# Optimization experiments

Hardware: AMD Instinct MI355X
Metric: run time of the kernel (lower is better)

The kernel has to match this reference:

```python
import jax, jax.numpy as jnp
import numpy as np

VAR_CXCY = 0.1   # SSD encoding variances
VAR_WH = 0.2
THRESH = 0.5     # match threshold from forward()
EPS = 1e-6


def point_form(p):
    """[P,4] (cx,cy,w,h) -> (x1,y1,x2,y2)."""
    return jnp.concatenate([p[..., :2] - p[..., 2:] / 2,
                            p[..., :2] + p[..., 2:] / 2], axis=-1)


def iou(a, b):
    """a: [N,4] xyxy, b: [P,4] xyxy -> [N,P] jaccard overlap."""
    lt = jnp.maximum(a[:, None, :2], b[None, :, :2])
    rb = jnp.minimum(a[:, None, 2:], b[None, :, 2:])
    wh = jnp.clip(rb - lt, 0.0)
    inter = wh[..., 0] * wh[..., 1]
    area_a = (a[:, 2] - a[:, 0]) * (a[:, 3] - a[:, 1])
    area_b = (b[:, 2] - b[:, 0]) * (b[:, 3] - b[:, 1])
    return inter / (area_a[:, None] + area_b[None, :] - inter + EPS)


def match_one(gt, labels, priors, priors_pt):
    """SSD match for a single image.
    gt: [N,4] xyxy, labels: [N] int, priors: [P,4] cxcywh, priors_pt: [P,4] xyxy.
    Returns loc targets [P,4] and conf targets [P] (0 = background).
    """
    ov = iou(gt, priors_pt)                       # [N,P]
    best_prior_idx = jnp.argmax(ov, axis=1)        # [N] best prior per gt
    best_truth_ov = jnp.max(ov, axis=0)            # [P]
    best_truth_idx = jnp.argmax(ov, axis=0)        # [P] best gt per prior
    n = gt.shape[0]
    # ensure every gt keeps its best prior
    best_truth_ov = best_truth_ov.at[best_prior_idx].set(2.0)
    best_truth_idx = best_truth_idx.at[best_prior_idx].set(jnp.arange(n))
    matches = gt[best_truth_idx]                   # [P,4]
    conf = labels[best_truth_idx] + 1              # shift so 0 = background
    conf = jnp.where(best_truth_ov < THRESH, 0, conf)
    # encode matched boxes relative to priors
    m_cxcy = (matches[:, :2] + matches[:, 2:]) * 0.5
    m_wh = jnp.clip(matches[:, 2:] - matches[:, :2], EPS)
    g_cxcy = (m_cxcy - priors[:, :2]) / (VAR_CXCY * priors[:, 2:])
    g_wh = jnp.log(m_wh / priors[:, 2:]) / VAR_WH
    return jnp.concatenate([g_cxcy, g_wh], axis=1), conf


def setup_inputs() -> dict:
    key = jax.random.key(0)
    k1, k2, k3, k4, k5 = jax.random.split(key, 5)
    B, N, P = 32, 100, 8732
    # ground-truth boxes: valid xyxy corners in [0,1]
    xy1 = jax.random.uniform(k1, (B, N, 2)) * 0.7
    wh = 0.05 + jax.random.uniform(k2, (B, N, 2)) * 0.25
    gt_boxes = jnp.concatenate([xy1, xy1 + wh], axis=-1).astype(jnp.float32)
    gt_labels = jax.random.randint(k3, (B, N), 0, 20)
    # priors: cxcywh
    p_cxcy = jax.random.uniform(k4, (P, 2))
    p_wh = 0.05 + jax.random.uniform(k5, (P, 2)) * 0.45
    priors = jnp.concatenate([p_cxcy, p_wh], axis=-1).astype(jnp.float32)
    return {"gt_boxes": gt_boxes, "gt_labels": gt_labels, "priors": priors}


def reference(gt_boxes, gt_labels, priors):
    priors_pt = point_form(priors)
    loc_t, conf_t = jax.vmap(
        lambda g, l: match_one(g, l, priors, priors_pt))(gt_boxes, gt_labels)
    return loc_t, conf_t
```

## Files before the change

### kernel.cpp

```cpp
#include <hip/hip_runtime.h>

#pragma clang fp contract(off)

#define BB 32
#define NN 100
#define PP 8732

__global__ __launch_bounds__(256) void k_iou_pass(
    const float* __restrict__ gt,
    const float* __restrict__ priors,
    unsigned long long* __restrict__ gkey,
    unsigned char* __restrict__ m8)
{
    __shared__ float4 s_gt[NN];
    __shared__ float  s_area[NN];
    __shared__ unsigned long long s_rk[4][NN];

    const int b    = blockIdx.y;
    const int t    = threadIdx.x;
    const int lane = t & 63;
    const int wid  = t >> 6;
    const int p    = blockIdx.x * 256 + t;
    const bool valid = p < PP;

    if (t < NN) {
        float4 g = reinterpret_cast<const float4*>(gt)[b * NN + t];
        s_gt[t] = g;
        s_area[t] = (g.z - g.x) * (g.w - g.y);
    }
    __syncthreads();

    const int pc = valid ? p : (PP - 1);
    const float4 pr = reinterpret_cast<const float4*>(priors)[pc];
    const float px1 = pr.x - pr.z * 0.5f;
    const float py1 = pr.y - pr.w * 0.5f;
    const float px2 = pr.x + pr.z * 0.5f;
    const float py2 = pr.y + pr.w * 0.5f;
    const float area_b = (px2 - px1) * (py2 - py1);

    float best_ov = -1.0f;
    int best_j = 0;

    #pragma unroll 2
    for (int j = 0; j < NN; ++j) {
        float4 g = s_gt[j];
        float ltx = fmaxf(g.x, px1), lty = fmaxf(g.y, py1);
        float rbx = fminf(g.z, px2), rby = fminf(g.w, py2);
        float w = fmaxf(rbx - ltx, 0.0f), h = fmaxf(rby - lty, 0.0f);
        float inter = w * h;
        float iou = inter / (s_area[j] + area_b - inter + 1e-6f);
        if (!valid) iou = -1.0f;

        if (iou > best_ov) { best_ov = iou; best_j = j; }

        float wm = iou;
        for (int off = 32; off; off >>= 1)
            wm = fmaxf(wm, __shfl_xor(wm, off));
        unsigned long long mask = __ballot(iou == wm);
        if (lane == __ffsll((unsigned long long)mask) - 1) {
            s_rk[wid][j] = (wm >= 0.0f)
                ? (((unsigned long long)__float_as_uint(wm) << 32) |
                   (unsigned int)(~p))
                : 0ull;
        }
    }
    __syncthreads();

    if (t < NN) {
        unsigned long long k0 = s_rk[0][t], k1 = s_rk[1][t];
        unsigned long long k2 = s_rk[2][t], k3 = s_rk[3][t];
        unsigned long long ka = k0 > k1 ? k0 : k1;
        unsigned long long kb = k2 > k3 ? k2 : k3;
        unsigned long long k  = ka > kb ? ka : kb;
        atomicMax(&gkey[b * NN + t], k);
    }
    if (valid) {
        m8[b * PP + p] =
            (unsigned char)(best_j | ((best_ov < 0.5f) ? 0x80 : 0));
    }
}

__global__ __launch_bounds__(256) void k_encode(
    const float* __restrict__ gt,
    const int*   __restrict__ labels,
    const float* __restrict__ priors,
    const unsigned long long* __restrict__ gkey,
    const unsigned char* __restrict__ m8,
    float* __restrict__ loc_out,
    float* __restrict__ conf_out)
{
    __shared__ float4 s_gt[NN];
    __shared__ int    s_lab[NN];
    __shared__ int    s_kp[NN];

    const int b = blockIdx.y;
    const int t = threadIdx.x;
    if (t < NN) {
        s_gt[t] = reinterpret_cast<const float4*>(gt)[b * NN + t];
        s_lab[t] = labels[b * NN + t];
        unsigned int lo = (unsigned int)(gkey[b * NN + t] & 0xFFFFFFFFull);
        s_kp[t] = (int)(~lo);
    }
    __syncthreads();

    const int p = blockIdx.x * 256 + t;
    if (p >= PP) return;

    int forced_j = -1;
    #pragma unroll 4
    for (int j = 0; j < NN; ++j)
        if (s_kp[j] == p) forced_j = j;

    const unsigned char m = m8[b * PP + p];
    const int j    = (forced_j >= 0) ? forced_j : (m & 0x7f);
    const int conf = (forced_j < 0 && (m & 0x80)) ? 0 : (s_lab[j] + 1);

    const float4 pr = reinterpret_cast<const float4*>(priors)[p];
    const float4 g  = s_gt[j];
    const float mcx = (g.x + g.z) * 0.5f;
    const float mcy = (g.y + g.w) * 0.5f;
    const float mw  = fmaxf(g.z - g.x, 1e-6f);
    const float mh  = fmaxf(g.w - g.y, 1e-6f);
    const float gcx = (mcx - pr.x) / (0.1f * pr.z);
    const float gcy = (mcy - pr.y) / (0.1f * pr.w);
    const float gw  = logf(mw / pr.z) / 0.2f;
    const float gh  = logf(mh / pr.w) / 0.2f;

    reinterpret_cast<float4*>(loc_out)[b * PP + p] =
        make_float4(gcx, gcy, gw, gh);
    conf_out[b * PP + p] = (float)conf;
}

extern "C" void kernel_launch(void* const* d_in, const int* in_sizes, int n_in,
                              void* d_out, int out_size, void* d_ws, size_t ws_size,
                              hipStream_t stream) {
    const float* gt     = (const float*)d_in[0];
    const int*   labels = (const int*)  d_in[1];
    const float* priors = (const float*)d_in[2];

    float* loc  = (float*)d_out;
    float* conf = (float*)d_out + (size_t)BB * PP * 4;

    unsigned long long* gkey = (unsigned long long*)d_ws;
    unsigned char* m8 = (unsigned char*)d_ws + (size_t)BB * NN * 8;

    hipMemsetAsync(gkey, 0, (size_t)BB * NN * 8, stream);

    dim3 grid((PP + 255) / 256, BB);
    k_iou_pass<<<grid, 256, 0, stream>>>(gt, priors, gkey, m8);
    k_encode<<<grid, 256, 0, stream>>>(gt, labels, priors, gkey, m8, loc, conf);
}
```

Baseline: 117.6 us.

## Replace per-gt wave shuffle reductions with chunked shared-memory IoU column reduction

The IoU pass no longer does a 6-step shuffle max plus ballot for each of the 100 ground-truth boxes. It writes IoU values for 16 gt boxes at a time into a padded shared-memory tile, then reduces each gt column with a two-level scan over 16-element segments, followed by an atomicMax. Ground-truth boxes are now read directly from global memory (uniform loads) rather than staged in shared memory, and the encode kernel likewise drops its shared-memory staging in favour of direct global reads. This trades shuffle and ballot work for extra barriers per chunk and serial shared-memory scans. Invalid priors now produce IoU 0 instead of -1, which relies on tie-breaking by prior index favouring valid lanes.

```diff
diff --git a/kernel.cpp b/kernel.cpp
--- a/kernel.cpp
+++ b/kernel.cpp
@@ -5,6 +5,8 @@
 #define BB 32
 #define NN 100
 #define PP 8732
+#define CH 16
+#define LDW 257
 
 __global__ __launch_bounds__(256) void k_iou_pass(
     const float* __restrict__ gt,
@@ -12,25 +14,15 @@
     unsigned long long* __restrict__ gkey,
     unsigned char* __restrict__ m8)
 {
-    __shared__ float4 s_gt[NN];
-    __shared__ float  s_area[NN];
-    __shared__ unsigned long long s_rk[4][NN];
+    __shared__ unsigned int s_iou[CH * LDW];
+    __shared__ unsigned long long s_part[CH][17];
 
-    const int b    = blockIdx.y;
-    const int t    = threadIdx.x;
-    const int lane = t & 63;
-    const int wid  = t >> 6;
-    const int p    = blockIdx.x * 256 + t;
+    const int b = blockIdx.y;
+    const int t = threadIdx.x;
+    const int p = blockIdx.x * 256 + t;
     const bool valid = p < PP;
+    const int pc = valid ? p : (PP - 1);
 
-    if (t < NN) {
-        float4 g = reinterpret_cast<const float4*>(gt)[b * NN + t];
-        s_gt[t] = g;
-        s_area[t] = (g.z - g.x) * (g.w - g.y);
-    }
-    __syncthreads();
-
-    const int pc = valid ? p : (PP - 1);
     const float4 pr = reinterpret_cast<const float4*>(priors)[pc];
     const float px1 = pr.x - pr.z * 0.5f;
     const float py1 = pr.y - pr.w * 0.5f;
@@ -38,42 +30,62 @@
     const float py2 = pr.y + pr.w * 0.5f;
     const float area_b = (px2 - px1) * (py2 - py1);
 
+    const float4* __restrict__ gtb =
+        reinterpret_cast<const float4*>(gt) + b * NN;
+
     float best_ov = -1.0f;
     int best_j = 0;
 
-    #pragma unroll 2
-    for (int j = 0; j < NN; ++j) {
-        float4 g = s_gt[j];
-        float ltx = fmaxf(g.x, px1), lty = fmaxf(g.y, py1);
-        float rbx = fminf(g.z, px2), rby = fminf(g.w, py2);
-        float w = fmaxf(rbx - ltx, 0.0f), h = fmaxf(rby - lty, 0.0f);
-        float inter = w * h;
-        float iou = inter / (s_area[j] + area_b - inter + 1e-6f);
-        if (!valid) iou = -1.0f;
+    for (int jc = 0; jc < NN; jc += CH) {
+        const int nr = min(NN - jc, CH);
 
-        if (iou > best_ov) { best_ov = iou; best_j = j; }
+        #pragma unroll 4
+        for (int jj = 0; jj < nr; ++jj) {
+            const int j = jc + jj;
+            float4 g = gtb[j];
+            float area_a = (g.z - g.x) * (g.w - g.y);
+            float ltx = fmaxf(g.x, px1), lty = fmaxf(g.y, py1);
+            float rbx = fminf(g.z, px2), rby = fminf(g.w, py2);
+            float w = fmaxf(rbx - ltx, 0.0f), h = fmaxf(rby - lty, 0.0f);
+            float inter = w * h;
+            float iou = inter / (area_a + area_b - inter + 1e-6f);
+            if (!valid) iou = 0.0f;
+            if (iou > best_ov) { best_ov = iou; best_j = j; }
+            s_iou[jj * LDW + t] = __float_as_uint(iou);
+        }
+        __syncthreads();
 
-        float wm = iou;
-        for (int off = 32; off; off >>= 1)
-            wm = fmaxf(wm, __shfl_xor(wm, off));
-        unsigned long long mask = __ballot(iou == wm);
-        if (lane == __ffsll((unsigned long long)mask) - 1) {
-            s_rk[wid][j] = (wm >= 0.0f)
-                ? (((unsigned long long)__float_as_uint(wm) << 32) |
-                   (unsigned int)(~p))
-                : 0ull;
+        {
+            const int r = t & 15;
+            const int s = t >> 4;
+            if (r < nr) {
+                const unsigned int* row = s_iou + r * LDW + s * 16;
+                unsigned int bb = row[0];
+                int bi = 0;
+                #pragma unroll
+                for (int i = 1; i < 16; ++i) {
+                    unsigned int v = row[i];
+                    if (v > bb) { bb = v; bi = i; }
+                }
+                int pw = blockIdx.x * 256 + s * 16 + bi;
+                s_part[r][s] = ((unsigned long long)bb << 32) |
+                               (unsigned int)(~pw);
+            }
         }
+        __syncthreads();
+
+        if (t < nr) {
+            unsigned long long best = s_part[t][0];
+            #pragma unroll
+            for (int s = 1; s < 16; ++s) {
+                unsigned long long k = s_part[t][s];
+                if (k > best) best = k;
+            }
+            atomicMax(&gkey[b * NN + jc + t], best);
+        }
+        __syncthreads();
     }
-    __syncthreads();
 
-    if (t < NN) {
-        unsigned long long k0 = s_rk[0][t], k1 = s_rk[1][t];
-        unsigned long long k2 = s_rk[2][t], k3 = s_rk[3][t];
-        unsigned long long ka = k0 > k1 ? k0 : k1;
-        unsigned long long kb = k2 > k3 ? k2 : k3;
-        unsigned long long k  = ka > kb ? ka : kb;
-        atomicMax(&gkey[b * NN + t], k);
-    }
     if (valid) {
         m8[b * PP + p] =
             (unsigned char)(best_j | ((best_ov < 0.5f) ? 0x80 : 0));
@@ -89,34 +101,27 @@
     float* __restrict__ loc_out,
     float* __restrict__ conf_out)
 {
-    __shared__ float4 s_gt[NN];
-    __shared__ int    s_lab[NN];
-    __shared__ int    s_kp[NN];
-
     const int b = blockIdx.y;
     const int t = threadIdx.x;
-    if (t < NN) {
-        s_gt[t] = reinterpret_cast<const float4*>(gt)[b * NN + t];
-        s_lab[t] = labels[b * NN + t];
-        unsigned int lo = (unsigned int)(gkey[b * NN + t] & 0xFFFFFFFFull);
-        s_kp[t] = (int)(~lo);
-    }
-    __syncthreads();
-
     const int p = blockIdx.x * 256 + t;
     if (p >= PP) return;
 
+    const unsigned long long* __restrict__ gk = gkey + b * NN;
+
     int forced_j = -1;
     #pragma unroll 4
-    for (int j = 0; j < NN; ++j)
-        if (s_kp[j] == p) forced_j = j;
+    for (int j = 0; j < NN; ++j) {
+        int kp = (int)~(unsigned int)(gk[j]);
+        if (kp == p) forced_j = j;
+    }
 
     const unsigned char m = m8[b * PP + p];
     const int j    = (forced_j >= 0) ? forced_j : (m & 0x7f);
-    const int conf = (forced_j < 0 && (m & 0x80)) ? 0 : (s_lab[j] + 1);
+    const int lab  = labels[b * NN + j];
+    const int conf = (forced_j < 0 && (m & 0x80)) ? 0 : (lab + 1);
 
     const float4 pr = reinterpret_cast<const float4*>(priors)[p];
-    const float4 g  = s_gt[j];
+    const float4 g  = reinterpret_cast<const float4*>(gt)[b * NN + j];
     const float mcx = (g.x + g.z) * 0.5f;
     const float mcy = (g.y + g.w) * 0.5f;
     const float mw  = fmaxf(g.z - g.x, 1e-6f);
```

Result: faster. 105.1 us (-10.6%).
